# Optimization experiments

Measured on AMD Instinct MI355X. Metric: run time of the kernel, lower is better.

## Reference

```python
import jax, jax.numpy as jnp
import numpy as np

VOL_SHAPE = (160, 192, 160)

def setup_inputs() -> dict:
    key = jax.random.key(0)
    k1, k2 = jax.random.split(key)
    vol = jax.random.normal(k1, (2, *VOL_SHAPE, 1), dtype=jnp.float32)
    trf = jax.random.normal(k2, (2, *VOL_SHAPE, 3), dtype=jnp.float32)
    return {"vol": vol, "trf": trf}

def _warp(vol, trf):
    # vol: [B, X, Y, Z, C]; trf: [B, X, Y, Z, 3] dense displacement field ('ij' indexing)
    B = vol.shape[0]
    shape = vol.shape[1:-1]
    nd = len(shape)
    # sample locations = identity grid + displacement
    grid = jnp.stack(jnp.meshgrid(*[jnp.arange(s, dtype=vol.dtype) for s in shape], indexing='ij'), axis=-1)
    loc = grid[None] + trf  # [B, X, Y, Z, 3]
    max_f = jnp.array([s - 1 for s in shape], dtype=vol.dtype)
    max_i = jnp.array([s - 1 for s in shape], dtype=jnp.int32)
    # fill_value=None -> clamp to volume border (voxelmorph interpn semantics)
    loc = jnp.clip(loc, 0.0, max_f)
    loc0f = jnp.floor(loc)
    loc0 = jnp.clip(loc0f.astype(jnp.int32), 0, max_i)        # lower corner indices
    loc1 = jnp.clip(loc0 + 1, 0, max_i)                       # upper corner indices (clipped)
    d1 = loc1.astype(vol.dtype) - loc                          # weight for lower corner
    d0 = 1.0 - d1                                              # weight for upper corner
    b = jnp.arange(B)[:, None, None, None]
    out = jnp.zeros(vol.shape, dtype=vol.dtype)
    for c in range(2 ** nd):                                   # 8 corners, fixed small loop
        bits = [(c >> d) & 1 for d in range(nd)]
        idx = [loc1[..., d] if bits[d] else loc0[..., d] for d in range(nd)]
        w = jnp.ones(loc.shape[:-1], dtype=vol.dtype)
        for d in range(nd):
            w = w * (d0[..., d] if bits[d] else d1[..., d])
        out = out + w[..., None] * vol[b, idx[0], idx[1], idx[2]]
    return out

def reference(vol, trf):
    return _warp(vol, trf)
```

## Files before the change

### kernel.cpp

```cpp
#include <hip/hip_runtime.h>


#define NXD 160
#define NYD 192
#define NZD 160
#define NVOX (NXD * NYD * NZD)
#define NBATCH 2

#define TXT 8
#define TYT 16
#define TZT 16
#define LXT 16
#define LYT 24
#define LZT 32
#define LDS_N (LXT * LYT * LZT)

#define TILES_X (NXD / TXT)
#define TILES_Y (NYD / TYT)
#define TILES_Z (NZD / TZT)
#define NBLOCKS (NBATCH * TILES_X * TILES_Y * TILES_Z)

typedef float f4 __attribute__((ext_vector_type(4)));

__global__ __launch_bounds__(512)
void warp3d_kernel(const float* __restrict__ vol,
                   const float* __restrict__ trf,
                   float* __restrict__ out) {
    __shared__ float tile[LDS_N];

    int bid = blockIdx.x;
    int tz = bid % TILES_Z;
    int r  = bid / TILES_Z;
    int ty = r % TILES_Y;
    int r2 = r / TILES_Y;
    int tx = r2 % TILES_X;
    int b  = r2 / TILES_X;

    int x0t = tx * TXT, y0t = ty * TYT, z0t = tz * TZT;
    int lox = x0t - 4, loy = y0t - 4, loz = z0t - 8;

    const float* vb = vol + (size_t)b * NVOX;

    int t = threadIdx.x;
    int zq = t & 3;
    int yq = (t >> 2) & 15;
    int xq = t >> 6;
    int x = x0t + xq, y = y0t + yq, zb0 = z0t + zq * 4;
    size_t vox_i = (((size_t)b * NXD + x) * NYD + y) * NZD + zb0;

    const f4* trfv = (const f4*)(trf + vox_i * 3);
    f4 t0 = trfv[0], t1 = trfv[1], t2 = trfv[2];

    bool interior = (lox >= 0) & (lox + LXT <= NXD) &
                    (loy >= 0) & (loy + LYT <= NYD) &
                    (loz >= 0) & (loz + LZT <= NZD);
    if (interior) {
        const float* gbase = vb + ((size_t)(lox * NYD + loy) * NZD + loz);
        int w = t >> 6;
        int l = t & 63;
#pragma unroll
        for (int it = 0; it < 6; ++it) {
            int chunk = it * 8 + w;
            int p = chunk * 256 + l * 4;
            int zi = p & 31;
            int rest = p >> 5;
            int yi = rest % LYT;
            int xi = rest / LYT;
            const float* g = gbase + (size_t)xi * (NYD * NZD) + yi * NZD + zi;
            __builtin_amdgcn_global_load_lds(
                (const __attribute__((address_space(1))) void*)g,
                (__attribute__((address_space(3))) void*)&tile[chunk * 256],
                16, 0, 0);
        }
    } else {
#pragma unroll 4
        for (int it = 0; it < LDS_N / 512; ++it) {
            int e = it * 512 + t;
            int zi = e & 31;
            int rest = e >> 5;
            int yi = rest % LYT;
            int xi = rest / LYT;
            int gx = min(max(lox + xi, 0), NXD - 1);
            int gy = min(max(loy + yi, 0), NYD - 1);
            int gz = min(max(loz + zi, 0), NZD - 1);
            tile[e] = vb[(size_t)(gx * NYD + gy) * NZD + gz];
        }
    }
    __syncthreads();

    float dxa[4] = {t0.x, t0.w, t1.z, t2.y};
    float dya[4] = {t0.y, t1.x, t1.w, t2.z};
    float dza[4] = {t0.z, t1.y, t2.x, t2.w};

    float res[4];
#pragma unroll
    for (int j = 0; j < 4; ++j) {
        float lx = fminf(fmaxf((float)x + dxa[j], 0.0f), (float)(NXD - 1));
        float ly = fminf(fmaxf((float)y + dya[j], 0.0f), (float)(NYD - 1));
        float lz = fminf(fmaxf((float)(zb0 + j) + dza[j], 0.0f), (float)(NZD - 1));
        float fx = floorf(lx), fy = floorf(ly), fz = floorf(lz);
        int x0 = (int)fx, y0 = (int)fy, z0 = (int)fz;
        float wx0 = fminf(fx + 1.0f, (float)(NXD - 1)) - lx;
        float wy0 = fminf(fy + 1.0f, (float)(NYD - 1)) - ly;
        float wz0 = fminf(fz + 1.0f, (float)(NZD - 1)) - lz;

        int ix = x0 - lox, iy = y0 - loy, iz = z0 - loz;
        bool ok = ((unsigned)ix <= LXT - 2) & ((unsigned)iy <= LYT - 2) &
                  ((unsigned)iz <= LZT - 2);
        int a = ok ? ((ix * LYT + iy) * LZT + iz) : 0;

        float v000 = tile[a],                   v001 = tile[a + 1];
        float v010 = tile[a + LZT],             v011 = tile[a + LZT + 1];
        float v100 = tile[a + LYT * LZT],       v101 = tile[a + LYT * LZT + 1];
        float v110 = tile[a + LYT * LZT + LZT], v111 = tile[a + LYT * LZT + LZT + 1];

        if (!ok) {
            int x1 = min(x0 + 1, NXD - 1);
            int y1 = min(y0 + 1, NYD - 1);
            int z1 = min(z0 + 1, NZD - 1);
            size_t o00 = (size_t)(x0 * NYD + y0) * NZD;
            size_t o01 = (size_t)(x0 * NYD + y1) * NZD;
            size_t o10 = (size_t)(x1 * NYD + y0) * NZD;
            size_t o11 = (size_t)(x1 * NYD + y1) * NZD;
            v000 = vb[o00 + z0]; v001 = vb[o00 + z1];
            v010 = vb[o01 + z0]; v011 = vb[o01 + z1];
            v100 = vb[o10 + z0]; v101 = vb[o10 + z1];
            v110 = vb[o11 + z0]; v111 = vb[o11 + z1];
        }

        float wx1 = 1.0f - wx0, wy1 = 1.0f - wy0, wz1 = 1.0f - wz0;
        res[j] = wx0 * (wy0 * (wz0 * v000 + wz1 * v001) +
                        wy1 * (wz0 * v010 + wz1 * v011)) +
                 wx1 * (wy0 * (wz0 * v100 + wz1 * v101) +
                        wy1 * (wz0 * v110 + wz1 * v111));
    }

    f4 o;
    o.x = res[0]; o.y = res[1]; o.z = res[2]; o.w = res[3];
    *(f4*)(out + vox_i) = o;
}

extern "C" void kernel_launch(void* const* d_in, const int* in_sizes, int n_in,
                              void* d_out, int out_size, void* d_ws, size_t ws_size,
                              hipStream_t stream) {
    const float* vol = (const float*)d_in[0];
    const float* trf = (const float*)d_in[1];
    float* out = (float*)d_out;

    warp3d_kernel<<<NBLOCKS, 512, 0, stream>>>(vol, trf, out);
}
```

Measured before the change: 223.5 us.

## Clamp halo tile origin to volume and XOR-swizzle LDS z layout

The tile origin is clamped so every block's halo lies fully inside the volume, which removes the slow scalar per-element fallback loop for border blocks; all blocks now use the async global_load_lds path. The z index inside each LDS row is XOR-swizzled by the y row to spread the trilinear gather reads across LDS banks and cut bank conflicts. Samples that fall outside the shifted tile still take the existing global-memory fallback, so correctness relies on that path. Extra index arithmetic is added per corner read.

```diff
diff --git a/kernel.cpp b/kernel.cpp
--- a/kernel.cpp
+++ b/kernel.cpp
@@ -37,7 +37,9 @@
     int b  = r2 / TILES_X;
 
     int x0t = tx * TXT, y0t = ty * TYT, z0t = tz * TZT;
-    int lox = x0t - 4, loy = y0t - 4, loz = z0t - 8;
+    int lox = min(max(x0t - 4, 0), NXD - LXT);
+    int loy = min(max(y0t - 4, 0), NYD - LYT);
+    int loz = min(max(z0t - 8, 0), NZD - LZT);
 
     const float* vb = vol + (size_t)b * NVOX;
 
@@ -51,39 +53,24 @@
     const f4* trfv = (const f4*)(trf + vox_i * 3);
     f4 t0 = trfv[0], t1 = trfv[1], t2 = trfv[2];
 
-    bool interior = (lox >= 0) & (lox + LXT <= NXD) &
-                    (loy >= 0) & (loy + LYT <= NYD) &
-                    (loz >= 0) & (loz + LZT <= NZD);
-    if (interior) {
+    {
         const float* gbase = vb + ((size_t)(lox * NYD + loy) * NZD + loz);
         int w = t >> 6;
         int l = t & 63;
+        int zgrp = (l & 7) << 2;
+        int lrow = l >> 3;
 #pragma unroll
         for (int it = 0; it < 6; ++it) {
             int chunk = it * 8 + w;
-            int p = chunk * 256 + l * 4;
-            int zi = p & 31;
-            int rest = p >> 5;
+            int rest = chunk * 8 + lrow;
             int yi = rest % LYT;
             int xi = rest / LYT;
-            const float* g = gbase + (size_t)xi * (NYD * NZD) + yi * NZD + zi;
+            int sz = zgrp ^ ((yi & 7) << 2);
+            const float* g = gbase + (size_t)xi * (NYD * NZD) + yi * NZD + sz;
             __builtin_amdgcn_global_load_lds(
                 (const __attribute__((address_space(1))) void*)g,
                 (__attribute__((address_space(3))) void*)&tile[chunk * 256],
                 16, 0, 0);
-        }
-    } else {
-#pragma unroll 4
-        for (int it = 0; it < LDS_N / 512; ++it) {
-            int e = it * 512 + t;
-            int zi = e & 31;
-            int rest = e >> 5;
-            int yi = rest % LYT;
-            int xi = rest / LYT;
-            int gx = min(max(lox + xi, 0), NXD - 1);
-            int gy = min(max(loy + yi, 0), NYD - 1);
-            int gz = min(max(loz + zi, 0), NZD - 1);
-            tile[e] = vb[(size_t)(gx * NYD + gy) * NZD + gz];
         }
     }
     __syncthreads();
@@ -107,12 +94,23 @@
         int ix = x0 - lox, iy = y0 - loy, iz = z0 - loz;
         bool ok = ((unsigned)ix <= LXT - 2) & ((unsigned)iy <= LYT - 2) &
                   ((unsigned)iz <= LZT - 2);
-        int a = ok ? ((ix * LYT + iy) * LZT + iz) : 0;
+        int sx = ok ? ix : 0;
+        int sy = ok ? iy : 0;
+        int sv = ok ? iz : 0;
 
-        float v000 = tile[a],                   v001 = tile[a + 1];
-        float v010 = tile[a + LZT],             v011 = tile[a + LZT + 1];
-        float v100 = tile[a + LYT * LZT],       v101 = tile[a + LYT * LZT + 1];
-        float v110 = tile[a + LYT * LZT + LZT], v111 = tile[a + LYT * LZT + LZT + 1];
+        int r00 = (sx * LYT + sy) * LZT;
+        int r01 = r00 + LZT;
+        int r10 = r00 + LYT * LZT;
+        int r11 = r10 + LZT;
+        int sw0 = (sy & 7) << 2;
+        int sw1 = ((sy + 1) & 7) << 2;
+        int za = sv ^ sw0, zb = (sv + 1) ^ sw0;
+        int zc = sv ^ sw1, zd = (sv + 1) ^ sw1;
+
+        float v000 = tile[r00 + za], v001 = tile[r00 + zb];
+        float v010 = tile[r01 + zc], v011 = tile[r01 + zd];
+        float v100 = tile[r10 + za], v101 = tile[r10 + zb];
+        float v110 = tile[r11 + zc], v111 = tile[r11 + zd];
 
         if (!ok) {
             int x1 = min(x0 + 1, NXD - 1);
```

After: 223.0 us. About the same (-0.2%).
